# Kernel tuning notes

Hardware: AMD Instinct MI355X
Metric: run time of the kernel (lower is better)

The kernel has to match this reference:

```python
import jax, jax.numpy as jnp
import numpy as np

N, E, C = 50000, 300000, 256  # nodes, edges, hidden size


def setup_inputs() -> dict:
    key = jax.random.key(0)
    ks = jax.random.split(key, 12)
    s = 0.05  # param init scale
    return {
        "x": jax.random.normal(ks[0], (N, C), dtype=jnp.float32),
        "edge_index": jax.random.randint(ks[1], (2, E), 0, N, dtype=jnp.int32),
        # GATConv layer 1 (heads=1): shared lin weight, att_src/att_dst vectors, bias
        "W1": jax.random.normal(ks[2], (C, C), dtype=jnp.float32) * s,
        "a1_src": jax.random.normal(ks[3], (C,), dtype=jnp.float32) * s,
        "a1_dst": jax.random.normal(ks[4], (C,), dtype=jnp.float32) * s,
        "b1": jnp.zeros((C,), dtype=jnp.float32),
        # GATConv layer 2
        "W2": jax.random.normal(ks[5], (C, C), dtype=jnp.float32) * s,
        "a2_src": jax.random.normal(ks[6], (C,), dtype=jnp.float32) * s,
        "a2_dst": jax.random.normal(ks[7], (C,), dtype=jnp.float32) * s,
        "b2": jnp.zeros((C,), dtype=jnp.float32),
        # Final Linear (torch convention: W [out, in], y = x @ W.T + b)
        "Wl": jax.random.normal(ks[8], (C, C), dtype=jnp.float32) * s,
        "bl": jnp.zeros((C,), dtype=jnp.float32),
    }


def _gat_conv(x, src, dst, W, a_src, a_dst, b):
    # PyG GATConv, heads=1, negative_slope=0.2, self-loops already appended.
    h = x @ W                                  # [N, C]
    alpha_src = h @ a_src                      # [N]
    alpha_dst = h @ a_dst                      # [N]
    e = jax.nn.leaky_relu(alpha_src[src] + alpha_dst[dst], 0.2)   # [E']
    # numerically stable softmax over incoming edges of each destination node
    m = jax.ops.segment_max(e, dst, num_segments=N)               # [N]
    ex = jnp.exp(e - m[dst])
    den = jax.ops.segment_sum(ex, dst, num_segments=N)            # [N]
    w = ex / den[dst]                                              # [E']
    out = jax.ops.segment_sum(h[src] * w[:, None], dst, num_segments=N)  # [N, C]
    return out + b


def reference(x, edge_index, W1, a1_src, a1_dst, b1, W2, a2_src, a2_dst, b2, Wl, bl):
    # add_self_loops (done inside each GATConv in PyG; appending once to the
    # input edge list is equivalent since both convs see the same edges)
    loops = jnp.arange(N, dtype=edge_index.dtype)
    ei = jnp.concatenate([edge_index, jnp.stack([loops, loops])], axis=1)
    src, dst = ei[0], ei[1]
    x = jax.nn.relu(_gat_conv(x, src, dst, W1, a1_src, a1_dst, b1))
    x = jax.nn.relu(_gat_conv(x, src, dst, W2, a2_src, a2_dst, b2))
    return x @ Wl.T + bl
```

## Files before the change

kernel.cpp:

```cpp
#include <hip/hip_runtime.h>

#define NN 50000
#define EE 300000
#define ET (EE + NN)
#define CD 256
#define PAD_M 50176
#define NB 196

typedef unsigned short ushortT;
typedef short bf16x8 __attribute__((ext_vector_type(8)));
typedef float f32x4 __attribute__((ext_vector_type(4)));

__device__ __forceinline__ ushortT f2b(float f) {
    unsigned u = __builtin_bit_cast(unsigned, f);
    unsigned r = (u + 0x7FFFu + ((u >> 16) & 1u)) >> 16;
    return (ushortT)r;
}
__device__ __forceinline__ float b2f(ushortT b) {
    return __builtin_bit_cast(float, ((unsigned)b) << 16);
}


__global__ __launch_bounds__(256) void wvec_kernel(
    const float* __restrict__ W1, const float* __restrict__ a1s,
    const float* __restrict__ a1d, const float* __restrict__ W2,
    const float* __restrict__ a2s, const float* __restrict__ a2d,
    float* __restrict__ w1s, float* __restrict__ w1d,
    float* __restrict__ w2s, float* __restrict__ w2d) {
    int b = blockIdx.x;
    const float* W = (b < 64) ? W1 : W2;
    const float* vs = (b < 64) ? a1s : a2s;
    const float* vd = (b < 64) ? a1d : a2d;
    float* os = (b < 64) ? w1s : w2s;
    float* od = (b < 64) ? w1d : w2d;
    int r = (b & 63) * 4 + (threadIdx.x >> 6);
    int lane = threadIdx.x & 63;
    float4 wv = *(const float4*)(W + (size_t)r * CD + lane * 4);
    float4 s4 = *(const float4*)(vs + lane * 4);
    float4 d4 = *(const float4*)(vd + lane * 4);
    float ss = wv.x * s4.x + wv.y * s4.y + wv.z * s4.z + wv.w * s4.w;
    float dd = wv.x * d4.x + wv.y * d4.y + wv.z * d4.z + wv.w * d4.w;
#pragma unroll
    for (int off = 1; off < 64; off <<= 1) {
        ss += __shfl_xor(ss, off);
        dd += __shfl_xor(dd, off);
    }
    if (lane == 0) {
        os[r] = ss;
        od[r] = dd;
    }
}

#define PREP_X 12500
#define PREP_W1 12564
#define PREP_W2 12628
#define PREP_WL 12692
#define PREP_END 12888

__global__ __launch_bounds__(256) void prep_kernel(
    const float* __restrict__ x, const float* __restrict__ W1,
    const float* __restrict__ W2, const float* __restrict__ Wl,
    ushortT* __restrict__ B0, ushortT* __restrict__ W1t,
    ushortT* __restrict__ W2t, ushortT* __restrict__ Wlt,
    int* __restrict__ deg, const float* __restrict__ w1s,
    const float* __restrict__ w1d, float* __restrict__ as1,
    float* __restrict__ ad1) {
    __shared__ float t[32][33];
    int b = blockIdx.x, tidx = threadIdx.x;
    if (b < PREP_X) {
        int node = b * 4 + (tidx >> 6);
        int lane = tidx & 63;
        float4 v = *(const float4*)(x + (size_t)node * CD + lane * 4);
        ushort4 o;
        o.x = f2b(v.x); o.y = f2b(v.y); o.z = f2b(v.z); o.w = f2b(v.w);
        *(ushort4*)(B0 + (size_t)node * CD + lane * 4) = o;
        float4 s4 = *(const float4*)(w1s + lane * 4);
        float4 d4 = *(const float4*)(w1d + lane * 4);
        float ss = v.x * s4.x + v.y * s4.y + v.z * s4.z + v.w * s4.w;
        float dd = v.x * d4.x + v.y * d4.y + v.z * d4.z + v.w * d4.w;
#pragma unroll
        for (int off = 1; off < 64; off <<= 1) {
            ss += __shfl_xor(ss, off);
            dd += __shfl_xor(dd, off);
        }
        if (lane == 0) {
            as1[node] = ss;
            ad1[node] = dd;
        }
    } else if (b < PREP_W2) {
        const float* W = (b < PREP_W1) ? W1 : W2;
        ushortT* Bt = (b < PREP_W1) ? W1t : W2t;
        int rel = b - ((b < PREP_W1) ? PREP_X : PREP_W1);
        int bx = (rel & 7) * 32;
        int by = (rel >> 3) * 32;
        int xx = tidx & 31, yy = tidx >> 5;
        for (int y = yy; y < 32; y += 8) t[y][xx] = W[(size_t)(bx + y) * CD + by + xx];
        __syncthreads();
        for (int y = yy; y < 32; y += 8)
            Bt[(size_t)(by + y) * CD + bx + xx] = f2b(t[xx][y]);
    } else if (b < PREP_WL) {
        int id = (b - PREP_W2) * 256 + tidx;
        float4 v = *(const float4*)(Wl + (size_t)id * 4);
        ushort4 o;
        o.x = f2b(v.x); o.y = f2b(v.y); o.z = f2b(v.z); o.w = f2b(v.w);
        *(ushort4*)(Wlt + (size_t)id * 4) = o;
    } else {
        int i = (b - PREP_WL) * 256 + tidx;
        if (i < NN) deg[i] = 1;
    }
}


__global__ void count_deg_kernel(const int* __restrict__ ei, int* __restrict__ deg) {
    int i = blockIdx.x * blockDim.x + threadIdx.x;
    if (i < EE) atomicAdd(&deg[ei[EE + i]], 1);
}

__global__ __launch_bounds__(256) void scan_part(const int* __restrict__ deg,
                                                 int* __restrict__ bsum) {
    int i = blockIdx.x * 256 + threadIdx.x;
    int v = (i < NN) ? deg[i] : 0;
#pragma unroll
    for (int off = 32; off > 0; off >>= 1) v += __shfl_down(v, off);
    __shared__ int w[4];
    if ((threadIdx.x & 63) == 0) w[threadIdx.x >> 6] = v;
    __syncthreads();
    if (threadIdx.x == 0) bsum[blockIdx.x] = w[0] + w[1] + w[2] + w[3];
}

__global__ __launch_bounds__(256) void scan_fill(const int* __restrict__ deg,
                                                 const int* __restrict__ bsum,
                                                 int* __restrict__ row_start,
                                                 int* __restrict__ fill_pos) {
    __shared__ int s[256];
    int t = threadIdx.x;
    int bv = (t < NB) ? bsum[t] : 0;
    s[t] = bv;
    __syncthreads();
    for (int off = 1; off < 256; off <<= 1) {
        int x = s[t];
        int y = (t >= off) ? s[t - off] : 0;
        __syncthreads();
        s[t] = x + y;
        __syncthreads();
    }
    int boff = s[blockIdx.x] - bsum[blockIdx.x];
    __syncthreads();
    int i = blockIdx.x * 256 + t;
    int v = (i < NN) ? deg[i] : 0;
    s[t] = v;
    __syncthreads();
    for (int off = 1; off < 256; off <<= 1) {
        int x = s[t];
        int y = (t >= off) ? s[t - off] : 0;
        __syncthreads();
        s[t] = x + y;
        __syncthreads();
    }
    int excl = s[t] - v + boff;
    if (i < NN) {
        row_start[i] = excl;
        fill_pos[i] = excl;
    }
    if (blockIdx.x == 0 && t == 0) row_start[NN] = ET;
}

__global__ void fill_csr_kernel(const int* __restrict__ ei, int* __restrict__ fill_pos,
                                int* __restrict__ srcs) {
    int i = blockIdx.x * blockDim.x + threadIdx.x;
    if (i < EE) {
        int s = ei[i];
        int d = ei[EE + i];
        int p = atomicAdd(&fill_pos[d], 1);
        srcs[p] = s;
    } else if (i < ET) {
        int n = i - EE;
        int p = atomicAdd(&fill_pos[n], 1);
        srcs[p] = n;
    }
}


template <int OUTF32>
__global__ __launch_bounds__(256, 4) void gemm_mfma(const ushortT* __restrict__ A,
                                                    const ushortT* __restrict__ Bt,
                                                    const float* __restrict__ bias,
                                                    float* __restrict__ outF,
                                                    ushortT* __restrict__ outB,
                                                    int M) {
    __shared__ ushortT Bs[64 * 256];
    int tid = threadIdx.x;
    int wave = tid >> 6, lane = tid & 63;
    int wm = wave * 32;
    int id = blockIdx.x;
    int bm = (id >> 2) * 128, bn = (id & 3) * 64;
    int l15 = lane & 15, quad = lane >> 4;

#pragma unroll
    for (int p = 0; p < 8; ++p) {
        int c = p * 256 + tid;
        int slot = c >> 5;
        int piece = c & 31;
        int col = (slot & 15) * 4 + (slot >> 4);
        int spiece = piece ^ (slot & 31);
        const ushortT* gb = Bt + (size_t)(bn + col) * CD + spiece * 8;
        __builtin_amdgcn_global_load_lds(
            (const __attribute__((address_space(1))) void*)gb,
            (__attribute__((address_space(3))) void*)(Bs + (size_t)(p * 256 + wave * 64) * 8),
            16, 0, 0);
    }

    bf16x8 a[2][8];
#pragma unroll
    for (int kk = 0; kk < 8; ++kk)
#pragma unroll
        for (int i = 0; i < 2; ++i)
            a[i][kk] = *(const bf16x8*)(A + (size_t)(bm + wm + i * 16 + l15) * CD + kk * 32 + quad * 8);

    __syncthreads();

    f32x4 acc[2][4] = {};

#pragma unroll
    for (int kk = 0; kk < 8; ++kk) {
        bf16x8 b[4];
        int kc = kk * 4 + quad;
#pragma unroll
        for (int j = 0; j < 4; ++j) {
            int slot = j * 16 + l15;
            b[j] = *(const bf16x8*)(Bs + (size_t)slot * 256 + (size_t)(kc ^ (slot & 31)) * 8);
        }
#pragma unroll
        for (int i = 0; i < 2; ++i)
#pragma unroll
            for (int j = 0; j < 4; ++j)
                acc[i][j] = __builtin_amdgcn_mfma_f32_16x16x32_bf16(a[i][kk], b[j], acc[i][j], 0, 0, 0);
    }

    int colb = bn + l15 * 4;
#pragma unroll
    for (int i = 0; i < 2; ++i) {
#pragma unroll
        for (int r = 0; r < 4; ++r) {
            int row = bm + wm + i * 16 + quad * 4 + r;
            if (OUTF32) {
                if (row < M) {
                    float4 bv = *(const float4*)(bias + colb);
                    float4 v;
                    v.x = acc[i][0][r] + bv.x;
                    v.y = acc[i][1][r] + bv.y;
                    v.z = acc[i][2][r] + bv.z;
                    v.w = acc[i][3][r] + bv.w;
                    *(float4*)(outF + (size_t)row * CD + colb) = v;
                }
            } else {
                ushort4 o;
                o.x = f2b(acc[i][0][r]);
                o.y = f2b(acc[i][1][r]);
                o.z = f2b(acc[i][2][r]);
                o.w = f2b(acc[i][3][r]);
                *(ushort4*)(outB + (size_t)row * CD + colb) = o;
            }
        }
    }
}


__device__ __forceinline__ float lrelu02(float x) { return x > 0.f ? x : 0.2f * x; }

template <int ALPHA2>
__global__ __launch_bounds__(256) void gat_agg(const ushortT* __restrict__ h,
                                               const float* __restrict__ as_,
                                               const float* __restrict__ ad_,
                                               const int* __restrict__ row_start,
                                               const int* __restrict__ srcs,
                                               const float* __restrict__ bias,
                                               ushortT* __restrict__ out,
                                               const float* __restrict__ w2s,
                                               const float* __restrict__ w2d,
                                               float* __restrict__ as_n,
                                               float* __restrict__ ad_n) {
    int node = blockIdx.x * 4 + (threadIdx.x >> 6);
    int lane = threadIdx.x & 63;
    if (node >= NN) return;
    int rs = row_start[node];
    int re = row_start[node + 1];
    int deg = re - rs;
    float adst = ad_[node];

    float a0 = 0.f, a1 = 0.f, a2 = 0.f, a3 = 0.f;

    if (deg <= 64) {
        int s_lane = srcs[rs + ((lane < deg) ? lane : 0)];
        float e = (lane < deg) ? lrelu02(as_[s_lane] + adst) : -1e30f;
        float m = e;
#pragma unroll
        for (int off = 1; off < 64; off <<= 1) m = fmaxf(m, __shfl_xor(m, off));
        float ex = (lane < deg) ? __expf(e - m) : 0.f;
        float den = ex;
#pragma unroll
        for (int off = 1; off < 64; off <<= 1) den += __shfl_xor(den, off);
        float wl = ex / den;

        for (int kk = 0; kk < deg; kk += 8) {
            int s[8];
            float w[8];
#pragma unroll
            for (int t = 0; t < 8; ++t) {
                int idx = kk + t;
                int ii = (idx < deg) ? idx : kk;
                int sv = __shfl(s_lane, ii);
                float wv = __shfl(wl, ii);
                s[t] = sv;
                w[t] = (idx < deg) ? wv : 0.f;
            }
            ushort4 hv[8];
#pragma unroll
            for (int t = 0; t < 8; ++t)
                hv[t] = *(const ushort4*)(h + (size_t)s[t] * CD + lane * 4);
#pragma unroll
            for (int t = 0; t < 8; ++t) {
                a0 += w[t] * b2f(hv[t].x);
                a1 += w[t] * b2f(hv[t].y);
                a2 += w[t] * b2f(hv[t].z);
                a3 += w[t] * b2f(hv[t].w);
            }
        }
    } else {
        float m = -1e30f;
        for (int k = rs + lane; k < re; k += 64) {
            float e = lrelu02(as_[srcs[k]] + adst);
            m = fmaxf(m, e);
        }
#pragma unroll
        for (int off = 1; off < 64; off <<= 1) m = fmaxf(m, __shfl_xor(m, off));
        float den = 0.f;
        for (int k = rs + lane; k < re; k += 64) {
            float e = lrelu02(as_[srcs[k]] + adst);
            den += __expf(e - m);
        }
#pragma unroll
        for (int off = 1; off < 64; off <<= 1) den += __shfl_xor(den, off);
        float inv_den = 1.f / den;
        for (int k = rs; k < re; ++k) {
            int s = srcs[k];
            float e = lrelu02(as_[s] + adst);
            float w = __expf(e - m) * inv_den;
            ushort4 hv = *(const ushort4*)(h + (size_t)s * CD + lane * 4);
            a0 += w * b2f(hv.x);
            a1 += w * b2f(hv.y);
            a2 += w * b2f(hv.z);
            a3 += w * b2f(hv.w);
        }
    }

    float4 b4 = *(const float4*)(bias + lane * 4);
    a0 = fmaxf(a0 + b4.x, 0.f);
    a1 = fmaxf(a1 + b4.y, 0.f);
    a2 = fmaxf(a2 + b4.z, 0.f);
    a3 = fmaxf(a3 + b4.w, 0.f);
    ushort4 o;
    o.x = f2b(a0);
    o.y = f2b(a1);
    o.z = f2b(a2);
    o.w = f2b(a3);
    *(ushort4*)(out + (size_t)node * CD + lane * 4) = o;

    if (ALPHA2) {
        float4 s4 = *(const float4*)(w2s + lane * 4);
        float4 d4 = *(const float4*)(w2d + lane * 4);
        float ss = a0 * s4.x + a1 * s4.y + a2 * s4.z + a3 * s4.w;
        float dd = a0 * d4.x + a1 * d4.y + a2 * d4.z + a3 * d4.w;
#pragma unroll
        for (int off = 1; off < 64; off <<= 1) {
            ss += __shfl_xor(ss, off);
            dd += __shfl_xor(dd, off);
        }
        if (lane == 0) {
            as_n[node] = ss;
            ad_n[node] = dd;
        }
    }
}


extern "C" void kernel_launch(void* const* d_in, const int* in_sizes, int n_in,
                              void* d_out, int out_size, void* d_ws, size_t ws_size,
                              hipStream_t stream) {
    const float* x = (const float*)d_in[0];
    const int* ei = (const int*)d_in[1];
    const float* W1 = (const float*)d_in[2];
    const float* a1s = (const float*)d_in[3];
    const float* a1d = (const float*)d_in[4];
    const float* b1 = (const float*)d_in[5];
    const float* W2 = (const float*)d_in[6];
    const float* a2s = (const float*)d_in[7];
    const float* a2d = (const float*)d_in[8];
    const float* b2 = (const float*)d_in[9];
    const float* Wl = (const float*)d_in[10];
    const float* bl = (const float*)d_in[11];
    float* out = (float*)d_out;

    char* w = (char*)d_ws;
    ushortT* B0 = (ushortT*)w; w += (size_t)PAD_M * CD * 2;
    ushortT* B1 = (ushortT*)w; w += (size_t)PAD_M * CD * 2;
    ushortT* B2 = (ushortT*)w; w += (size_t)PAD_M * CD * 2;
    ushortT* W1t = (ushortT*)w; w += (size_t)CD * CD * 2;
    ushortT* W2t = (ushortT*)w; w += (size_t)CD * CD * 2;
    ushortT* Wlt = (ushortT*)w; w += (size_t)CD * CD * 2;
    float* as1 = (float*)w; w += (size_t)NN * 4;
    float* ad1 = (float*)w; w += (size_t)NN * 4;
    float* as2 = (float*)w; w += (size_t)NN * 4;
    float* ad2 = (float*)w; w += (size_t)NN * 4;
    float* w1s = (float*)w; w += CD * 4;
    float* w1d = (float*)w; w += CD * 4;
    float* w2s = (float*)w; w += CD * 4;
    float* w2d = (float*)w; w += CD * 4;
    int* deg = (int*)w; w += (size_t)NN * 4;
    int* fill_pos = (int*)w; w += (size_t)NN * 4;
    int* srcs = (int*)w; w += (size_t)ET * 4;
    int* bsum = (int*)w; w += 1024;
    int* row_start = (int*)w; w += (size_t)(NN + 1) * 4;

    wvec_kernel<<<128, 256, 0, stream>>>(W1, a1s, a1d, W2, a2s, a2d,
                                         w1s, w1d, w2s, w2d);

    prep_kernel<<<PREP_END, 256, 0, stream>>>(x, W1, W2, Wl, B0, W1t, W2t, Wlt,
                                              deg, w1s, w1d, as1, ad1);

    count_deg_kernel<<<(EE + 255) / 256, 256, 0, stream>>>(ei, deg);
    scan_part<<<NB, 256, 0, stream>>>(deg, bsum);
    scan_fill<<<NB, 256, 0, stream>>>(deg, bsum, row_start, fill_pos);
    fill_csr_kernel<<<(ET + 255) / 256, 256, 0, stream>>>(ei, fill_pos, srcs);

    int ggrid = (PAD_M / 128) * 4;
    int nwave_blocks = (NN + 3) / 4;

    gemm_mfma<0><<<ggrid, 256, 0, stream>>>(B0, W1t, nullptr, nullptr, B1, NN);
    gat_agg<1><<<nwave_blocks, 256, 0, stream>>>(B1, as1, ad1, row_start, srcs,
                                                 b1, B2, w2s, w2d, as2, ad2);

    gemm_mfma<0><<<ggrid, 256, 0, stream>>>(B2, W2t, nullptr, nullptr, B1, NN);
    gat_agg<0><<<nwave_blocks, 256, 0, stream>>>(B1, as2, ad2, row_start, srcs,
                                                 b2, B0, nullptr, nullptr,
                                                 nullptr, nullptr);

    gemm_mfma<1><<<ggrid, 256, 0, stream>>>(B0, Wlt, bl, out, nullptr, NN);
}
```

Measured before the change: 295.3 us.

## Process two nodes per wavefront with 16-byte bf16 gathers in GAT aggregation

```diff
diff --git a/kernel.cpp b/kernel.cpp
--- a/kernel.cpp
+++ b/kernel.cpp
@@ -280,103 +280,111 @@
                                                const float* __restrict__ w2d,
                                                float* __restrict__ as_n,
                                                float* __restrict__ ad_n) {
-    int node = blockIdx.x * 4 + (threadIdx.x >> 6);
-    int lane = threadIdx.x & 63;
+    int node = blockIdx.x * 8 + (threadIdx.x >> 5);
+    int hl = threadIdx.x & 31;
     if (node >= NN) return;
     int rs = row_start[node];
     int re = row_start[node + 1];
     int deg = re - rs;
     float adst = ad_[node];
 
-    float a0 = 0.f, a1 = 0.f, a2 = 0.f, a3 = 0.f;
-
-    if (deg <= 64) {
-        int s_lane = srcs[rs + ((lane < deg) ? lane : 0)];
-        float e = (lane < deg) ? lrelu02(as_[s_lane] + adst) : -1e30f;
+    float acc[8] = {0.f, 0.f, 0.f, 0.f, 0.f, 0.f, 0.f, 0.f};
+
+    int maxdeg = max(deg, __shfl_xor(deg, 32));
+
+    if (maxdeg <= 32) {
+        int s_lane = srcs[rs + ((hl < deg) ? hl : 0)];
+        float e = (hl < deg) ? lrelu02(as_[s_lane] + adst) : -1e30f;
         float m = e;
 #pragma unroll
-        for (int off = 1; off < 64; off <<= 1) m = fmaxf(m, __shfl_xor(m, off));
-        float ex = (lane < deg) ? __expf(e - m) : 0.f;
+        for (int off = 1; off < 32; off <<= 1) m = fmaxf(m, __shfl_xor(m, off));
+        float ex = (hl < deg) ? __expf(e - m) : 0.f;
         float den = ex;
 #pragma unroll
-        for (int off = 1; off < 64; off <<= 1) den += __shfl_xor(den, off);
+        for (int off = 1; off < 32; off <<= 1) den += __shfl_xor(den, off);
         float wl = ex / den;
 
-        for (int kk = 0; kk < deg; kk += 8) {
+        for (int kk = 0; kk < maxdeg; kk += 8) {
             int s[8];
             float w[8];
 #pragma unroll
             for (int t = 0; t < 8; ++t) {
                 int idx = kk + t;
-                int ii = (idx < deg) ? idx : kk;
-                int sv = __shfl(s_lane, ii);
-                float wv = __shfl(wl, ii);
+                int ii = (idx < deg) ? idx : 0;
+                int sv = __shfl(s_lane, ii, 32);
+                float wv = __shfl(wl, ii, 32);
                 s[t] = sv;
                 w[t] = (idx < deg) ? wv : 0.f;
             }
-            ushort4 hv[8];
+            bf16x8 hv[8];
 #pragma unroll
             for (int t = 0; t < 8; ++t)
-                hv[t] = *(const ushort4*)(h + (size_t)s[t] * CD + lane * 4);
+                hv[t] = *(const bf16x8*)(h + (size_t)s[t] * CD + hl * 8);
 #pragma unroll
             for (int t = 0; t < 8; ++t) {
-                a0 += w[t] * b2f(hv[t].x);
-                a1 += w[t] * b2f(hv[t].y);
-                a2 += w[t] * b2f(hv[t].z);
-                a3 += w[t] * b2f(hv[t].w);
+#pragma unroll
+                for (int c = 0; c < 8; ++c)
+                    acc[c] += w[t] * b2f((ushortT)hv[t][c]);
             }
         }
     } else {
         float m = -1e30f;
-        for (int k = rs + lane; k < re; k += 64) {
+        for (int k = rs + hl; k < re; k += 32) {
             float e = lrelu02(as_[srcs[k]] + adst);
             m = fmaxf(m, e);
         }
 #pragma unroll
-        for (int off = 1; off < 64; off <<= 1) m = fmaxf(m, __shfl_xor(m, off));
+        for (int off = 1; off < 32; off <<= 1) m = fmaxf(m, __shfl_xor(m, off));
         float den = 0.f;
-        for (int k = rs + lane; k < re; k += 64) {
+        for (int k = rs + hl; k < re; k += 32) {
             float e = lrelu02(as_[srcs[k]] + adst);
             den += __expf(e - m);
         }
 #pragma unroll
-        for (int off = 1; off < 64; off <<= 1) den += __shfl_xor(den, off);
+        for (int off = 1; off < 32; off <<= 1) den += __shfl_xor(den, off);
         float inv_den = 1.f / den;
         for (int k = rs; k < re; ++k) {
-            int s = srcs[k];
-            float e = lrelu02(as_[s] + adst);
-            float w = __expf(e - m) * inv_den;
-            ushort4 hv = *(const ushort4*)(h + (size_t)s * CD + lane * 4);
-            a0 += w * b2f(hv.x);
-            a1 += w * b2f(hv.y);
-            a2 += w * b2f(hv.z);
-            a3 += w * b2f(hv.w);
-        }
-    }
-
-    float4 b4 = *(const float4*)(bias + lane * 4);
-    a0 = fmaxf(a0 + b4.x, 0.f);
-    a1 = fmaxf(a1 + b4.y, 0.f);
-    a2 = fmaxf(a2 + b4.z, 0.f);
-    a3 = fmaxf(a3 + b4.w, 0.f);
-    ushort4 o;
-    o.x = f2b(a0);
-    o.y = f2b(a1);
-    o.z = f2b(a2);
-    o.w = f2b(a3);
-    *(ushort4*)(out + (size_t)node * CD + lane * 4) = o;
+            int sv = srcs[k];
+            float e = lrelu02(as_[sv] + adst);
+            float wv = __expf(e - m) * inv_den;
+            bf16x8 hv = *(const bf16x8*)(h + (size_t)sv * CD + hl * 8);
+#pragma unroll
+            for (int c = 0; c < 8; ++c)
+                acc[c] += wv * b2f((ushortT)hv[c]);
+        }
+    }
+
+    float4 bv0 = *(const float4*)(bias + hl * 8);
+    float4 bv1 = *(const float4*)(bias + hl * 8 + 4);
+    float r[8];
+    r[0] = fmaxf(acc[0] + bv0.x, 0.f);
+    r[1] = fmaxf(acc[1] + bv0.y, 0.f);
+    r[2] = fmaxf(acc[2] + bv0.z, 0.f);
+    r[3] = fmaxf(acc[3] + bv0.w, 0.f);
+    r[4] = fmaxf(acc[4] + bv1.x, 0.f);
+    r[5] = fmaxf(acc[5] + bv1.y, 0.f);
+    r[6] = fmaxf(acc[6] + bv1.z, 0.f);
+    r[7] = fmaxf(acc[7] + bv1.w, 0.f);
+    bf16x8 o;
+#pragma unroll
+    for (int c = 0; c < 8; ++c) o[c] = (short)f2b(r[c]);
+    *(bf16x8*)(out + (size_t)node * CD + hl * 8) = o;
 
     if (ALPHA2) {
-        float4 s4 = *(const float4*)(w2s + lane * 4);
-        float4 d4 = *(const float4*)(w2d + lane * 4);
-        float ss = a0 * s4.x + a1 * s4.y + a2 * s4.z + a3 * s4.w;
-        float dd = a0 * d4.x + a1 * d4.y + a2 * d4.z + a3 * d4.w;
-#pragma unroll
-        for (int off = 1; off < 64; off <<= 1) {
+        float4 s0 = *(const float4*)(w2s + hl * 8);
+        float4 s1 = *(const float4*)(w2s + hl * 8 + 4);
+        float4 d0 = *(const float4*)(w2d + hl * 8);
+        float4 d1 = *(const float4*)(w2d + hl * 8 + 4);
+        float ss = r[0] * s0.x + r[1] * s0.y + r[2] * s0.z + r[3] * s0.w +
+                   r[4] * s1.x + r[5] * s1.y + r[6] * s1.z + r[7] * s1.w;
+        float dd = r[0] * d0.x + r[1] * d0.y + r[2] * d0.z + r[3] * d0.w +
+                   r[4] * d1.x + r[5] * d1.y + r[6] * d1.z + r[7] * d1.w;
+#pragma unroll
+        for (int off = 1; off < 32; off <<= 1) {
             ss += __shfl_xor(ss, off);
             dd += __shfl_xor(dd, off);
         }
-        if (lane == 0) {
+        if (hl == 0) {
             as_n[node] = ss;
             ad_n[node] = dd;
         }
@@ -434,16 +442,16 @@
     fill_csr_kernel<<<(ET + 255) / 256, 256, 0, stream>>>(ei, fill_pos, srcs);
 
     int ggrid = (PAD_M / 128) * 4;
-    int nwave_blocks = (NN + 3) / 4;
+    int nagg_blocks = (NN + 7) / 8;
 
     gemm_mfma<0><<<ggrid, 256, 0, stream>>>(B0, W1t, nullptr, nullptr, B1, NN);
-    gat_agg<1><<<nwave_blocks, 256, 0, stream>>>(B1, as1, ad1, row_start, srcs,
-                                                 b1, B2, w2s, w2d, as2, ad2);
+    gat_agg<1><<<nagg_blocks, 256, 0, stream>>>(B1, as1, ad1, row_start, srcs,
+                                                b1, B2, w2s, w2d, as2, ad2);
 
     gemm_mfma<0><<<ggrid, 256, 0, stream>>>(B2, W2t, nullptr, nullptr, B1, NN);
-    gat_agg<0><<<nwave_blocks, 256, 0, stream>>>(B1, as2, ad2, row_start, srcs,
-                                                 b2, B0, nullptr, nullptr,
-                                                 nullptr, nullptr);
+    gat_agg<0><<<nagg_blocks, 256, 0, stream>>>(B1, as2, ad2, row_start, srcs,
+                                                b2, B0, nullptr, nullptr,
+                                                nullptr, nullptr);
 
     gemm_mfma<1><<<ggrid, 256, 0, stream>>>(B0, Wlt, bl, out, nullptr, NN);
 }
```

Measured after the change: 290.1 us. Within noise of the previous version (-1.8%).
